# Performance work log

Measured on AMD Instinct MI355X. Metric: run time of the kernel, lower is better.

## Reference

```python
import jax, jax.numpy as jnp
import numpy as np

EPS = 1e-6

def setup_inputs() -> dict:
    key = jax.random.key(0)
    k1, k2 = jax.random.split(key)
    B, M, N, D = 4, 4096, 4096, 64
    input_features = jax.random.uniform(k1, (B, N, D), dtype=jnp.float32)
    input_associations = jax.random.uniform(k2, (B, M, N), dtype=jnp.float32)
    return {"input_features": input_features, "input_associations": input_associations}

def reference(input_features, input_associations):
    # feat: [B, N, D], assoc: [B, M, N]
    assoc_safe = input_associations + EPS
    assoc_norm = assoc_safe / jnp.sum(assoc_safe, axis=2, keepdims=True)  # normalize over N
    # weighted aggregation == batched matmul: [B,M,N] @ [B,N,D] -> [B,M,D]
    return jnp.einsum('bmn,bnd->bmd', assoc_norm, input_features)
```

## Files before the change

### kernel.cpp

```cpp
#include <hip/hip_runtime.h>

constexpr int Bn = 4;
constexpr int Mm = 4096;
constexpr int Nn = 4096;
constexpr int Dd = 64;
#define EPS_VAL 1e-6f

typedef __attribute__((ext_vector_type(8))) short short8_t;
typedef __attribute__((ext_vector_type(4))) float floatx4;

__device__ __forceinline__ unsigned short f32_to_bf16_rne(float x) {
    unsigned u = __float_as_uint(x);
    unsigned r = u + 0x7FFFu + ((u >> 16) & 1u);
    return (unsigned short)(r >> 16);
}

__global__ __launch_bounds__(256) void transpose_feat_kernel(
    const float* __restrict__ feat, unsigned short* __restrict__ ft)
{
    __shared__ unsigned short tile[64][66];
    const int b  = blockIdx.x >> 6;
    const int n0 = (blockIdx.x & 63) * 64;
    const int t  = threadIdx.x;
    const int row = t >> 2;
    const int seg = t & 3;

    const float* src = feat + ((size_t)(b * Nn + n0 + row)) * Dd + seg * 16;
    #pragma unroll
    for (int v = 0; v < 4; ++v) {
        float4 f = ((const float4*)src)[v];
        tile[row][seg * 16 + v * 4 + 0] = f32_to_bf16_rne(f.x);
        tile[row][seg * 16 + v * 4 + 1] = f32_to_bf16_rne(f.y);
        tile[row][seg * 16 + v * 4 + 2] = f32_to_bf16_rne(f.z);
        tile[row][seg * 16 + v * 4 + 3] = f32_to_bf16_rne(f.w);
    }
    __syncthreads();

    const int d    = row;
    const int nseg = seg;
    short8_t v0, v1;
    #pragma unroll
    for (int i = 0; i < 8; ++i) v0[i] = (short)tile[nseg * 16 + i][d];
    #pragma unroll
    for (int i = 0; i < 8; ++i) v1[i] = (short)tile[nseg * 16 + 8 + i][d];

    unsigned short* dst = ft + ((size_t)(b * Dd + d)) * Nn + n0 + nseg * 16;
    *(short8_t*)(dst)     = v0;
    *(short8_t*)(dst + 8) = v1;
}

__global__ __launch_bounds__(256, 1) void agg_kernel(
    const float* __restrict__ assoc, const unsigned short* __restrict__ ft,
    float* __restrict__ out)
{
    const int b  = blockIdx.x >> 6;
    const int mt = blockIdx.x & 63;
    const int w  = threadIdx.x >> 6;
    const int l  = threadIdx.x & 63;
    const int q  = l >> 4;
    const int mi = l & 15;
    const int m0 = mt * 64 + w * 16;

    const float* aptr = assoc + ((size_t)b * Mm + (size_t)(m0 + mi)) * Nn + q * 8;
    const unsigned short* fptr = ft + (size_t)b * Dd * Nn + (size_t)mi * Nn + q * 8;

    floatx4 acc0 = {0.f, 0.f, 0.f, 0.f};
    floatx4 acc1 = acc0, acc2 = acc0, acc3 = acc0;
    float s0 = 0.f, s1 = 0.f;

    #pragma unroll 4
    for (int k0 = 0; k0 < Nn; k0 += 32) {
        float4 alo = *(const float4*)(aptr + k0);
        float4 ahi = *(const float4*)(aptr + k0 + 4);
        float av[8] = {alo.x, alo.y, alo.z, alo.w, ahi.x, ahi.y, ahi.z, ahi.w};

        short8_t afrag;
        #pragma unroll
        for (int j = 0; j < 8; ++j) {
            unsigned short h = f32_to_bf16_rne(av[j] + EPS_VAL);
            afrag[j] = (short)h;
            float hv = __uint_as_float(((unsigned)h) << 16);
            if (j & 1) s1 += hv; else s0 += hv;
        }

        short8_t bf0 = *(const short8_t*)(fptr + k0);
        short8_t bf1 = *(const short8_t*)(fptr + k0 + 16 * Nn);
        short8_t bf2 = *(const short8_t*)(fptr + k0 + 32 * Nn);
        short8_t bf3 = *(const short8_t*)(fptr + k0 + 48 * Nn);

        acc0 = __builtin_amdgcn_mfma_f32_16x16x32_bf16(afrag, bf0, acc0, 0, 0, 0);
        acc1 = __builtin_amdgcn_mfma_f32_16x16x32_bf16(afrag, bf1, acc1, 0, 0, 0);
        acc2 = __builtin_amdgcn_mfma_f32_16x16x32_bf16(afrag, bf2, acc2, 0, 0, 0);
        acc3 = __builtin_amdgcn_mfma_f32_16x16x32_bf16(afrag, bf3, acc3, 0, 0, 0);
    }

    float s = s0 + s1;
    s += __shfl_xor(s, 16);
    s += __shfl_xor(s, 32);

    #pragma unroll
    for (int r = 0; r < 4; ++r) {
        float Sr  = __shfl(s, q * 4 + r);
        float inv = 1.0f / Sr;
        size_t base = ((size_t)b * Mm + (size_t)(m0 + q * 4 + r)) * Dd + mi;
        out[base +  0] = acc0[r] * inv;
        out[base + 16] = acc1[r] * inv;
        out[base + 32] = acc2[r] * inv;
        out[base + 48] = acc3[r] * inv;
    }
}

extern "C" void kernel_launch(void* const* d_in, const int* in_sizes, int n_in,
                              void* d_out, int out_size, void* d_ws, size_t ws_size,
                              hipStream_t stream) {
    const float* feat  = (const float*)d_in[0];
    const float* assoc = (const float*)d_in[1];
    float* out = (float*)d_out;
    unsigned short* ft = (unsigned short*)d_ws;

    hipLaunchKernelGGL(transpose_feat_kernel, dim3(Bn * (Nn / 64)), dim3(256), 0, stream,
                       feat, ft);
    hipLaunchKernelGGL(agg_kernel, dim3(Bn * (Mm / 64)), dim3(256), 0, stream,
                       assoc, ft, out);
}
```

Baseline: 383.2 us.

## Split N reduction across waves with LDS reduction and quadruple block count

Each block now handles 16 rows of M rather than 64, and its four waves each cover a quarter of the N dimension. The partial MFMA accumulators and row sums are combined through shared memory before normalisation and store. The grid grows from 256 to 1024 blocks, with launch bounds raised to allow 4 blocks per CU. This is meant to fill more CUs and hide the latency of the memory-bound assoc stream, at the cost of an LDS reduction, a block barrier, and more register pressure.

```diff
diff --git a/kernel.cpp b/kernel.cpp
--- a/kernel.cpp
+++ b/kernel.cpp
@@ -49,27 +49,28 @@
     *(short8_t*)(dst + 8) = v1;
 }
 
-__global__ __launch_bounds__(256, 1) void agg_kernel(
+__global__ __launch_bounds__(256, 4) void agg_kernel(
     const float* __restrict__ assoc, const unsigned short* __restrict__ ft,
     float* __restrict__ out)
 {
-    const int b  = blockIdx.x >> 6;
-    const int mt = blockIdx.x & 63;
+    constexpr int KW = Nn / 4;
+    const int b  = blockIdx.x >> 8;
+    const int mt = blockIdx.x & 255;
+    const int m0 = mt * 16;
     const int w  = threadIdx.x >> 6;
     const int l  = threadIdx.x & 63;
     const int q  = l >> 4;
     const int mi = l & 15;
-    const int m0 = mt * 64 + w * 16;
 
-    const float* aptr = assoc + ((size_t)b * Mm + (size_t)(m0 + mi)) * Nn + q * 8;
-    const unsigned short* fptr = ft + (size_t)b * Dd * Nn + (size_t)mi * Nn + q * 8;
+    const float* aptr = assoc + ((size_t)b * Mm + (size_t)(m0 + mi)) * Nn + w * KW + q * 8;
+    const unsigned short* fptr = ft + (size_t)b * Dd * Nn + (size_t)mi * Nn + w * KW + q * 8;
 
     floatx4 acc0 = {0.f, 0.f, 0.f, 0.f};
     floatx4 acc1 = acc0, acc2 = acc0, acc3 = acc0;
     float s0 = 0.f, s1 = 0.f;
 
     #pragma unroll 4
-    for (int k0 = 0; k0 < Nn; k0 += 32) {
+    for (int k0 = 0; k0 < KW; k0 += 32) {
         float4 alo = *(const float4*)(aptr + k0);
         float4 ahi = *(const float4*)(aptr + k0 + 4);
         float av[8] = {alo.x, alo.y, alo.z, alo.w, ahi.x, ahi.y, ahi.z, ahi.w};
@@ -98,15 +99,31 @@
     s += __shfl_xor(s, 16);
     s += __shfl_xor(s, 32);
 
+    __shared__ float lds_acc[4][4][64][4];
+    __shared__ float lds_s[4][16];
+
+    *(float4*)&lds_acc[w][0][l][0] = make_float4(acc0[0], acc0[1], acc0[2], acc0[3]);
+    *(float4*)&lds_acc[w][1][l][0] = make_float4(acc1[0], acc1[1], acc1[2], acc1[3]);
+    *(float4*)&lds_acc[w][2][l][0] = make_float4(acc2[0], acc2[1], acc2[2], acc2[3]);
+    *(float4*)&lds_acc[w][3][l][0] = make_float4(acc3[0], acc3[1], acc3[2], acc3[3]);
+    if (l < 16) lds_s[w][l] = s;
+    __syncthreads();
+
+    float4 a0 = *(float4*)&lds_acc[0][w][l][0];
+    float4 a1 = *(float4*)&lds_acc[1][w][l][0];
+    float4 a2 = *(float4*)&lds_acc[2][w][l][0];
+    float4 a3 = *(float4*)&lds_acc[3][w][l][0];
+    float accf[4] = {a0.x + a1.x + a2.x + a3.x,
+                     a0.y + a1.y + a2.y + a3.y,
+                     a0.z + a1.z + a2.z + a3.z,
+                     a0.w + a1.w + a2.w + a3.w};
+
     #pragma unroll
     for (int r = 0; r < 4; ++r) {
-        float Sr  = __shfl(s, q * 4 + r);
-        float inv = 1.0f / Sr;
-        size_t base = ((size_t)b * Mm + (size_t)(m0 + q * 4 + r)) * Dd + mi;
-        out[base +  0] = acc0[r] * inv;
-        out[base + 16] = acc1[r] * inv;
-        out[base + 32] = acc2[r] * inv;
-        out[base + 48] = acc3[r] * inv;
+        const int row = q * 4 + r;
+        float S = lds_s[0][row] + lds_s[1][row] + lds_s[2][row] + lds_s[3][row];
+        float inv = 1.0f / S;
+        out[((size_t)b * Mm + (size_t)(m0 + row)) * Dd + w * 16 + mi] = accf[r] * inv;
     }
 }
 
@@ -120,6 +137,6 @@
 
     hipLaunchKernelGGL(transpose_feat_kernel, dim3(Bn * (Nn / 64)), dim3(256), 0, stream,
                        feat, ft);
-    hipLaunchKernelGGL(agg_kernel, dim3(Bn * (Mm / 64)), dim3(256), 0, stream,
+    hipLaunchKernelGGL(agg_kernel, dim3(Bn * (Mm / 16)), dim3(256), 0, stream,
                        assoc, ft, out);
 }
```

Measured after the change: 401.4 us. 1.05x slower.
